# Kernel optimization log

Hardware: AMD Instinct MI355X
Metric: run time of the kernel (lower is better)

Reference implementation:

```python
import jax, jax.numpy as jnp
import numpy as np

G = 8
EPS = 1e-5

def conv3d(x, w, stride=1, padding=0, bias=None):
    out = jax.lax.conv_general_dilated(
        x, w, (stride,) * 3, [(padding, padding)] * 3,
        dimension_numbers=('NCDHW', 'OIDHW', 'NCDHW'))
    if bias is not None:
        out = out + bias.reshape(1, -1, 1, 1, 1)
    return out

def batchnorm(x, g, b):
    mu = x.mean(axis=(0, 2, 3, 4), keepdims=True)
    var = x.var(axis=(0, 2, 3, 4), keepdims=True)
    return (x - mu) * jax.lax.rsqrt(var + EPS) * g.reshape(1, -1, 1, 1, 1) + b.reshape(1, -1, 1, 1, 1)

def up2_trilinear_ac(x):
    # trilinear upsample x2, align_corners=True
    def interp(a, axis):
        n = a.shape[axis]; m = 2 * n
        src = jnp.arange(m, dtype=a.dtype) * ((n - 1) / (m - 1))
        i0 = jnp.floor(src).astype(jnp.int32)
        i1 = jnp.minimum(i0 + 1, n - 1)
        w = src - i0.astype(a.dtype)
        a0 = jnp.take(a, i0, axis=axis)
        a1 = jnp.take(a, i1, axis=axis)
        shp = [1] * a.ndim; shp[axis] = m
        w = w.reshape(shp)
        return a0 * (1 - w) + a1 * w
    for ax in (2, 3, 4):
        x = interp(x, ax)
    return x

def double_conv_up(x, c1, g1, b1, c2, g2, b2):
    x = jax.nn.relu(batchnorm(conv3d(x, c1, padding=1), g1, b1))
    x = up2_trilinear_ac(x)
    x = jax.nn.relu(batchnorm(conv3d(x, c2, padding=1), g2, b2))
    return x

def correlation_3d(prev, nxt):
    # FunctionCorrelation_3D: 3 z-edge-masked copies of prev x 9 (dx,dy) shifts of next
    N, C, X, Y, Z = prev.shape
    zslab = jnp.zeros_like(prev[..., :1])
    pm = [jnp.concatenate([prev[..., :-1], zslab], -1),  # k=-1: last z slice zeroed
          prev,                                          # k=0
          jnp.concatenate([zslab, prev[..., 1:]], -1)]   # k=+1: first z slice zeroed
    npad = jnp.pad(nxt, [(0, 0), (0, 0), (1, 1), (1, 1), (0, 0)])
    ns = [npad[:, :, 1 + di:1 + di + X, 1 + dj:1 + dj + Y, :]
          for di in (-1, 0, 1) for dj in (-1, 0, 1)]
    chans = [(pm[k] * ns[s]).mean(axis=1) for k in range(3) for s in range(9)]
    return jnp.stack(chans, axis=1)  # [N,27,X,Y,Z]

def fwd_diff(a, axis):
    hi = jax.lax.slice_in_dim(a, 1, a.shape[axis], axis=axis)
    zero = jnp.zeros_like(jax.lax.slice_in_dim(a, 0, 1, axis=axis))
    return jnp.concatenate([hi, zero], axis=axis) - a

def cgrid_to_motion(u, v, w, shape):
    mu = 0.5 * (u[:, :, 1:-1, 1:-1, 1:] + u[:, :, 1:-1, 1:-1, :-1])
    mv = 0.5 * (v[:, :, 1:-1, 1:, 1:-1] + v[:, :, 1:-1, :-1, 1:-1])
    mw = 0.5 * (w[:, :, 1:, 1:-1, 1:-1] + w[:, :, :-1, 1:-1, 1:-1])
    m = jnp.concatenate([mu, mv, mw], axis=1)
    H, W, T = shape
    up = (m.shape[2] - H) // 2; left = (m.shape[3] - W) // 2; front = (m.shape[4] - T) // 2
    return m[:, :, up:up + H, left:left + W, front:front + T]

def calc_phi_velocity(phi, shape):
    u = fwd_diff(phi, 4)[:, :, :, :, :-1]
    v = fwd_diff(phi, 3)[:, :, :, :-1, :]
    w = fwd_diff(phi, 2)[:, :, :-1, :, :]
    return cgrid_to_motion(u, v, w, shape)

def calc_stream_velocity(s, shape):
    s0, s1, s2 = s[:, 0:1], s[:, 1:2], s[:, 2:3]
    u = (fwd_diff(s1, 2) - fwd_diff(s0, 3))[:, :, :, :, :-1]
    v = (fwd_diff(s0, 4) - fwd_diff(s2, 2))[:, :, :, :-1, :]
    w = (fwd_diff(s2, 3) - fwd_diff(s1, 4))[:, :, :-1, :, :]
    return cgrid_to_motion(u, v, w, shape)

def trilinear_sample(tex, px, py, pz):
    N, C, X, Y, Z = tex.shape
    px = jnp.clip(px, 0.0, X - 1.0); py = jnp.clip(py, 0.0, Y - 1.0); pz = jnp.clip(pz, 0.0, Z - 1.0)
    x0 = jnp.floor(px).astype(jnp.int32); y0 = jnp.floor(py).astype(jnp.int32); z0 = jnp.floor(pz).astype(jnp.int32)
    x1 = jnp.minimum(x0 + 1, X - 1); y1 = jnp.minimum(y0 + 1, Y - 1); z1 = jnp.minimum(z0 + 1, Z - 1)
    fx = (px - x0.astype(px.dtype))[:, None]
    fy = (py - y0.astype(py.dtype))[:, None]
    fz = (pz - z0.astype(pz.dtype))[:, None]
    tf = tex.reshape(N, C, X * Y * Z)
    def gather(xi, yi, zi):
        idx = ((xi * Y + yi) * Z + zi).reshape(N, 1, -1)
        idx = jnp.broadcast_to(idx, (N, C, X * Y * Z))
        return jnp.take_along_axis(tf, idx, axis=2).reshape(N, C, X, Y, Z)
    c = ((gather(x0, y0, z0) * (1 - fx) + gather(x1, y0, z0) * fx) * (1 - fy)
         + (gather(x0, y1, z0) * (1 - fx) + gather(x1, y1, z0) * fx) * fy) * (1 - fz) \
        + ((gather(x0, y0, z1) * (1 - fx) + gather(x1, y0, z1) * fx) * (1 - fy)
           + (gather(x0, y1, z1) * (1 - fx) + gather(x1, y1, z1) * fx) * fy) * fz
    return c

def bfecc_warp(tex, vel):
    # vel channel 0 -> z (last axis), 1 -> y, 2 -> x displacements
    N, C, X, Y, Z = tex.shape
    gx, gy, gz = jnp.meshgrid(jnp.arange(X, dtype=tex.dtype),
                              jnp.arange(Y, dtype=tex.dtype),
                              jnp.arange(Z, dtype=tex.dtype), indexing='ij')
    def advect(f, v):
        return trilinear_sample(f, gx[None] - v[:, 2], gy[None] - v[:, 1], gz[None] - v[:, 0])
    phi1 = advect(tex, vel)
    phi2 = advect(phi1, -vel)
    return advect(tex + 0.5 * (tex - phi2), vel)

def helm_forward(P):
    prev, nxt, texture = P['prev'], P['next'], P['texture']
    mask, boundary = P['mask'], P['boundary']
    B, C, H, W, T = prev.shape
    shape = texture.shape[-3:]
    pm = (prev * mask).reshape(B * G, C // G, H, W, T)
    pb = (prev * boundary).reshape(B * G, C // G, H, W, T)
    nm = (nxt * mask).reshape(B * G, C // G, H, W, T)
    f_pm = conv3d(pm, P['enc_w'], stride=2, bias=P['enc_b'])
    f_pb = conv3d(pb, P['enc_w'], stride=2, bias=P['enc_b'])
    f_nm = conv3d(nm, P['enc_w'], stride=2, bias=P['enc_b'])
    corr = jnp.concatenate([correlation_3d(f_pm, f_nm), correlation_3d(f_pb, f_nm)], axis=1)
    phi = double_conv_up(corr, P['phi_c1_w'], P['phi_bn1_g'], P['phi_bn1_b'],
                         P['phi_c2_w'], P['phi_bn2_g'], P['phi_bn2_b'])
    phi = conv3d(phi, P['phi_out_w'], bias=P['phi_out_b']) * P['phi_weight']
    vort = double_conv_up(corr, P['vort_c1_w'], P['vort_bn1_g'], P['vort_bn1_b'],
                          P['vort_c2_w'], P['vort_bn2_g'], P['vort_bn2_b'])
    vort = conv3d(vort, P['vort_out_w'], bias=P['vort_out_b']) * P['vort_weight'] * nxt.shape[-2]
    helmholtz = jnp.concatenate([phi, vort], axis=1)  # [B*G,4,H,W,T]
    vel_phi = calc_phi_velocity(helmholtz[:, 0:1], shape)
    vel_vort = calc_stream_velocity(helmholtz[:, 1:4], shape)
    vel = vel_phi + vel_vort
    Bt, Ct, Ht, Wt, Tt = texture.shape
    tex_g = texture.reshape(Bt * G, Ct // G, Ht, Wt, Tt)
    pred = bfecc_warp(tex_g, vel).reshape(Bt, Ct, Ht, Wt, Tt)
    h = jnp.moveaxis(pred, 1, -1)
    mu = h.mean(-1, keepdims=True); var = h.var(-1, keepdims=True)
    h = (h - mu) * jax.lax.rsqrt(var + EPS) * P['ln_g'] + P['ln_b']
    h = jax.nn.gelu(h @ P['ff_w1'] + P['ff_b1'], approximate=False) @ P['ff_w2'] + P['ff_b2']
    x = pred + jnp.moveaxis(h, -1, 1)
    return x, helmholtz, vel, vel_phi, vel_vort

def setup_inputs() -> dict:
    key = jax.random.key(0)
    ks = jax.random.split(key, 16)
    D = 64
    inp = {
        'prev': jax.random.normal(ks[0], (1, D, 66, 66, 66), jnp.float32),
        'next': jax.random.normal(ks[1], (1, D, 66, 66, 66), jnp.float32),
        'texture': jax.random.normal(ks[2], (1, D, 64, 64, 64), jnp.float32),
        'mask': jax.random.uniform(ks[3], (1, 1, 66, 66, 66), jnp.float32),
        'boundary': jax.random.uniform(ks[4], (1, 1, 66, 66, 66), jnp.float32),
        'enc_w': 0.02 * jax.random.normal(ks[5], (D, D // G, 2, 2, 2), jnp.float32),
        'enc_b': jnp.zeros((D,), jnp.float32),
        'phi_c1_w': 0.02 * jax.random.normal(ks[6], (8, 54, 3, 3, 3), jnp.float32),
        'phi_bn1_g': jnp.ones((8,), jnp.float32), 'phi_bn1_b': jnp.zeros((8,), jnp.float32),
        'phi_c2_w': 0.02 * jax.random.normal(ks[7], (8, 8, 3, 3, 3), jnp.float32),
        'phi_bn2_g': jnp.ones((8,), jnp.float32), 'phi_bn2_b': jnp.zeros((8,), jnp.float32),
        'phi_out_w': 0.02 * jax.random.normal(ks[8], (1, 8, 1, 1, 1), jnp.float32),
        'phi_out_b': jnp.zeros((1,), jnp.float32),
        'vort_c1_w': 0.02 * jax.random.normal(ks[9], (8, 54, 3, 3, 3), jnp.float32),
        'vort_bn1_g': jnp.ones((8,), jnp.float32), 'vort_bn1_b': jnp.zeros((8,), jnp.float32),
        'vort_c2_w': 0.02 * jax.random.normal(ks[10], (8, 8, 3, 3, 3), jnp.float32),
        'vort_bn2_g': jnp.ones((8,), jnp.float32), 'vort_bn2_b': jnp.zeros((8,), jnp.float32),
        'vort_out_w': 0.02 * jax.random.normal(ks[11], (3, 8, 1, 1, 1), jnp.float32),
        'vort_out_b': jnp.zeros((3,), jnp.float32),
        'phi_weight': jnp.array([0.5], jnp.float32),
        'vort_weight': jnp.array([0.1], jnp.float32),
        'ln_g': jnp.ones((D,), jnp.float32), 'ln_b': jnp.zeros((D,), jnp.float32),
        'ff_w1': 0.02 * jax.random.normal(ks[12], (D, D), jnp.float32),
        'ff_b1': jnp.zeros((D,), jnp.float32),
        'ff_w2': 0.02 * jax.random.normal(ks[13], (D, D), jnp.float32),
        'ff_b2': jnp.zeros((D,), jnp.float32),
    }
    return inp

def reference(prev, next, texture, mask, boundary, enc_w, enc_b,
              phi_c1_w, phi_bn1_g, phi_bn1_b, phi_c2_w, phi_bn2_g, phi_bn2_b, phi_out_w, phi_out_b,
              vort_c1_w, vort_bn1_g, vort_bn1_b, vort_c2_w, vort_bn2_g, vort_bn2_b, vort_out_w, vort_out_b,
              phi_weight, vort_weight, ln_g, ln_b, ff_w1, ff_b1, ff_w2, ff_b2):
    P = dict(prev=prev, next=next, texture=texture, mask=mask, boundary=boundary,
             enc_w=enc_w, enc_b=enc_b,
             phi_c1_w=phi_c1_w, phi_bn1_g=phi_bn1_g, phi_bn1_b=phi_bn1_b,
             phi_c2_w=phi_c2_w, phi_bn2_g=phi_bn2_g, phi_bn2_b=phi_bn2_b,
             phi_out_w=phi_out_w, phi_out_b=phi_out_b,
             vort_c1_w=vort_c1_w, vort_bn1_g=vort_bn1_g, vort_bn1_b=vort_bn1_b,
             vort_c2_w=vort_c2_w, vort_bn2_g=vort_bn2_g, vort_bn2_b=vort_bn2_b,
             vort_out_w=vort_out_w, vort_out_b=vort_out_b,
             phi_weight=phi_weight, vort_weight=vort_weight,
             ln_g=ln_g, ln_b=ln_b, ff_w1=ff_w1, ff_b1=ff_b1, ff_w2=ff_w2, ff_b2=ff_b2)
    return helm_forward(P)
```

## Files before the change

kernel.cpp:

```cpp
#include <hip/hip_runtime.h>
#include <math.h>

constexpr int S1 = 66, S1_2 = S1*S1, S1_3 = S1*S1*S1;
constexpr int S2 = 33, S2_2 = S2*S2, S2_3 = S2*S2*S2;
constexpr int S3 = 64, S3_2 = S3*S3, S3_3 = S3*S3*S3;
constexpr int NG = 8;
constexpr int CG = 8;
constexpr int D  = 64;

constexpr size_t X_OFF     = 0;
constexpr size_t HELM_OFF  = (size_t)D*S3_3;
constexpr size_t VEL_OFF   = HELM_OFF + (size_t)NG*4*S1_3;
constexpr size_t VPHI_OFF  = VEL_OFF  + (size_t)NG*3*S3_3;
constexpr size_t VVORT_OFF = VPHI_OFF + (size_t)NG*3*S3_3;

constexpr size_t CORR_OFF  = 0;
constexpr size_t C1P_OFF   = CORR_OFF + (size_t)NG*54*S2_3;
constexpr size_t C1V_OFF   = C1P_OFF  + (size_t)NG*8*S2_3;
constexpr size_t STATS_OFF = C1V_OFF  + (size_t)NG*8*S2_3;

constexpr int NBLK_STAT = 256;

__global__ void __launch_bounds__(256)
enc_kernel(const float* __restrict__ in, const float* __restrict__ msk,
           const float* __restrict__ w,  const float* __restrict__ b,
           float* __restrict__ out) {
    int pos = blockIdx.x*256 + threadIdx.x;
    int g = blockIdx.y;
    if (pos >= S2_3) return;
    int x = pos / S2_2, rem = pos % S2_2, y = rem / S2, z = rem % S2;
    int ib = 2*x*S1_2 + 2*y*S1 + 2*z;
    float mv[8];
#pragma unroll
    for (int c = 0; c < 8; ++c) {
        int dx = c>>2, dy = (c>>1)&1, dz = c&1;
        mv[c] = msk[ib + dx*S1_2 + dy*S1 + dz];
    }
    float mi[64];
#pragma unroll
    for (int ic = 0; ic < 8; ++ic) {
        const float* inc = in + (size_t)(g*CG + ic)*S1_3 + ib;
#pragma unroll
        for (int c = 0; c < 8; ++c) {
            int dx = c>>2, dy = (c>>1)&1, dz = c&1;
            mi[ic*8 + c] = inc[dx*S1_2 + dy*S1 + dz] * mv[c];
        }
    }
    for (int oc = 0; oc < 64; ++oc) {
        float acc = b[oc];
#pragma unroll
        for (int t = 0; t < 64; ++t) acc = fmaf(mi[t], w[oc*64 + t], acc);
        out[(size_t)(g*64 + oc)*S2_3 + pos] = acc;
    }
}

__global__ void __launch_bounds__(256)
corr_kernel(const float* __restrict__ fpv, const float* __restrict__ fnv,
            float* __restrict__ corr, int base_ch) {
    int pos = blockIdx.x*256 + threadIdx.x;
    int g = blockIdx.y;
    if (pos >= S2_3) return;
    int x = pos / S2_2, rem = pos % S2_2, y = rem / S2, z = rem % S2;
    const float* fp = fpv + (size_t)g*64*S2_3;
    const float* fn = fnv + (size_t)g*64*S2_3;
    int   nidx[9];
    float nmask[9];
#pragma unroll
    for (int di = -1; di <= 1; ++di) {
        int xx = x + di; int xc = min(max(xx,0),S2-1); bool okx = (unsigned)xx < (unsigned)S2;
#pragma unroll
        for (int dj = -1; dj <= 1; ++dj) {
            int yy = y + dj; int yc = min(max(yy,0),S2-1);
            bool ok = okx && ((unsigned)yy < (unsigned)S2);
            nidx [(di+1)*3 + dj+1] = xc*S2_2 + yc*S2 + z;
            nmask[(di+1)*3 + dj+1] = ok ? 1.f : 0.f;
        }
    }
    float acc[9] = {0,0,0,0,0,0,0,0,0};
    for (int c = 0; c < 64; ++c) {
        float pc = fp[(size_t)c*S2_3 + pos];
        const float* fnc = fn + (size_t)c*S2_3;
#pragma unroll
        for (int s = 0; s < 9; ++s) acc[s] = fmaf(pc, fnc[nidx[s]]*nmask[s], acc[s]);
    }
    const float inv64 = 1.f/64.f;
#pragma unroll
    for (int k = 0; k < 3; ++k) {
        float zf = ((k==0 && z==S2-1) || (k==2 && z==0)) ? 0.f : inv64;
#pragma unroll
        for (int s = 0; s < 9; ++s)
            corr[(size_t)(g*54 + base_ch + k*9 + s)*S2_3 + pos] = acc[s]*zf;
    }
}

template<int NIC, int S_>
__global__ void __launch_bounds__(256)
conv3_kernel(const float* __restrict__ in, const float* __restrict__ w,
             float* __restrict__ out) {
    constexpr int SS = S_*S_, SSS = S_*S_*S_;
    int pos = blockIdx.x*256 + threadIdx.x;
    int g = blockIdx.y;
    if (pos >= SSS) return;
    int x = pos / SS, rem = pos % SS, y = rem / S_, z = rem % S_;
    float acc[8] = {0,0,0,0,0,0,0,0};
    for (int ic = 0; ic < NIC; ++ic) {
        const float* inc = in + (size_t)(g*NIC + ic)*SSS;
        float v[27];
#pragma unroll
        for (int dx = -1; dx <= 1; ++dx) {
            int xx = x + dx; int xc = min(max(xx,0),S_-1); bool okx = (unsigned)xx < (unsigned)S_;
#pragma unroll
            for (int dy = -1; dy <= 1; ++dy) {
                int yy = y + dy; int yc = min(max(yy,0),S_-1);
                bool oky = okx && ((unsigned)yy < (unsigned)S_);
#pragma unroll
                for (int dz = -1; dz <= 1; ++dz) {
                    int zz = z + dz; int zc = min(max(zz,0),S_-1);
                    bool ok = oky && ((unsigned)zz < (unsigned)S_);
                    float t = inc[xc*SS + yc*S_ + zc];
                    v[(dx+1)*9 + (dy+1)*3 + (dz+1)] = ok ? t : 0.f;
                }
            }
        }
#pragma unroll
        for (int oc = 0; oc < 8; ++oc) {
            const float* wr = w + (size_t)(oc*NIC + ic)*27;
#pragma unroll
            for (int t = 0; t < 27; ++t) acc[oc] = fmaf(v[t], wr[t], acc[oc]);
        }
    }
#pragma unroll
    for (int oc = 0; oc < 8; ++oc)
        out[(size_t)(g*8 + oc)*SSS + pos] = acc[oc];
}

__global__ void __launch_bounds__(256)
bn_part_kernel(const float* __restrict__ in, int npos, double* __restrict__ part) {
    int ch = blockIdx.y;
    int blk = blockIdx.x;
    int tid = threadIdx.x;
    double s = 0.0, ss = 0.0;
    for (int g = 0; g < NG; ++g) {
        const float* p = in + (size_t)(g*8 + ch)*npos;
        for (int i = blk*256 + tid; i < npos; i += NBLK_STAT*256) {
            double v = p[i]; s += v; ss += v*v;
        }
    }
    __shared__ double sd[256], sd2[256];
    sd[tid] = s; sd2[tid] = ss; __syncthreads();
    for (int o = 128; o > 0; o >>= 1) {
        if (tid < o) { sd[tid] += sd[tid+o]; sd2[tid] += sd2[tid+o]; }
        __syncthreads();
    }
    if (tid == 0) {
        part[((size_t)ch*NBLK_STAT + blk)*2    ] = sd[0];
        part[((size_t)ch*NBLK_STAT + blk)*2 + 1] = sd2[0];
    }
}

__global__ void __launch_bounds__(256)
bn_finish_kernel(const double* __restrict__ part, int npos, float* __restrict__ stats) {
    int ch = blockIdx.x;
    int tid = threadIdx.x;
    __shared__ double sd[256], sd2[256];
    sd[tid]  = part[((size_t)ch*NBLK_STAT + tid)*2];
    sd2[tid] = part[((size_t)ch*NBLK_STAT + tid)*2 + 1];
    __syncthreads();
    for (int o = 128; o > 0; o >>= 1) {
        if (tid < o) { sd[tid] += sd[tid+o]; sd2[tid] += sd2[tid+o]; }
        __syncthreads();
    }
    if (tid == 0) {
        double n = (double)npos * NG;
        double mean = sd[0]/n;
        double var  = sd2[0]/n - mean*mean;
        stats[ch*2]   = (float)mean;
        stats[ch*2+1] = (float)(1.0/sqrt(var + 1e-5));
    }
}

__global__ void __launch_bounds__(256)
bn_relu_up_kernel(const float* __restrict__ in, const float* __restrict__ stats,
                  const float* __restrict__ gamma, const float* __restrict__ beta,
                  float* __restrict__ out) {
    int pos = blockIdx.x*256 + threadIdx.x;
    if (pos >= S1_3) return;
    int gc = blockIdx.y;
    int ch = gc & 7;
    int X = pos / S1_2, rem = pos % S1_2, Y = rem / S1, Z = rem % S1;
    const float scale = (float)(32.0/65.0);
    float sx = (float)X*scale, sy = (float)Y*scale, sz = (float)Z*scale;
    int x0 = (int)floorf(sx), y0 = (int)floorf(sy), z0 = (int)floorf(sz);
    float wx = sx - (float)x0, wy = sy - (float)y0, wz = sz - (float)z0;
    int x1 = min(x0+1, S2-1), y1 = min(y0+1, S2-1), z1 = min(z0+1, S2-1);
    float a = stats[ch*2+1]*gamma[ch];
    float c = beta[ch] - stats[ch*2]*a;
    const float* p = in + (size_t)gc*S2_3;
    auto val = [&](int xi, int yi, int zi) {
        float t = fmaf(p[xi*S2_2 + yi*S2 + zi], a, c);
        return t > 0.f ? t : 0.f;
    };
    float t00 = val(x0,y0,z0)*(1.f-wx) + val(x1,y0,z0)*wx;
    float t10 = val(x0,y1,z0)*(1.f-wx) + val(x1,y1,z0)*wx;
    float t01 = val(x0,y0,z1)*(1.f-wx) + val(x1,y0,z1)*wx;
    float t11 = val(x0,y1,z1)*(1.f-wx) + val(x1,y1,z1)*wx;
    float u0 = t00*(1.f-wy) + t10*wy;
    float u1 = t01*(1.f-wy) + t11*wy;
    out[(size_t)gc*S1_3 + pos] = u0*(1.f-wz) + u1*wz;
}

template<int NOC>
__global__ void __launch_bounds__(256)
outconv_kernel(const float* __restrict__ in, const float* __restrict__ stats,
               const float* __restrict__ gamma, const float* __restrict__ beta,
               const float* __restrict__ ow, const float* __restrict__ ob,
               const float* __restrict__ wscale, float extra,
               float* __restrict__ helm, int oc_off) {
    int pos = blockIdx.x*256 + threadIdx.x;
    int g = blockIdx.y;
    if (pos >= S1_3) return;
    float r[8];
#pragma unroll
    for (int ic = 0; ic < 8; ++ic) {
        float a = stats[ic*2+1]*gamma[ic];
        float c = beta[ic] - stats[ic*2]*a;
        float t = fmaf(in[(size_t)(g*8 + ic)*S1_3 + pos], a, c);
        r[ic] = t > 0.f ? t : 0.f;
    }
    float sc = wscale[0]*extra;
#pragma unroll
    for (int oc = 0; oc < NOC; ++oc) {
        float acc = ob[oc];
#pragma unroll
        for (int ic = 0; ic < 8; ++ic) acc = fmaf(r[ic], ow[oc*8 + ic], acc);
        helm[(size_t)(g*4 + oc_off + oc)*S1_3 + pos] = acc*sc;
    }
}

__global__ void __launch_bounds__(256)
velocity_kernel(const float* __restrict__ helm, float* __restrict__ vel,
                float* __restrict__ vphi, float* __restrict__ vvort) {
    int pos = blockIdx.x*256 + threadIdx.x;
    int g = blockIdx.y;
    if (pos >= S3_3) return;
    int x = pos / S3_2, rem = pos % S3_2, y = rem / S3, z = rem % S3;
    const float* H = helm + (size_t)g*4*S1_3;
    auto idx = [&](int c, int i, int j, int k) { return (size_t)c*S1_3 + i*S1_2 + j*S1 + k; };
    float pu = 0.5f*(H[idx(0,x+1,y+1,z+2)] - H[idx(0,x+1,y+1,z  )]);
    float pv = 0.5f*(H[idx(0,x+1,y+2,z+1)] - H[idx(0,x+1,y  ,z+1)]);
    float pw = 0.5f*(H[idx(0,x+2,y+1,z+1)] - H[idx(0,x  ,y+1,z+1)]);
    float vu = 0.5f*( (H[idx(2,x+2,y+1,z+1)]-H[idx(2,x+1,y+1,z+1)]) - (H[idx(1,x+1,y+2,z+1)]-H[idx(1,x+1,y+1,z+1)])
                    + (H[idx(2,x+2,y+1,z  )]-H[idx(2,x+1,y+1,z  )]) - (H[idx(1,x+1,y+2,z  )]-H[idx(1,x+1,y+1,z  )]) );
    float vv = 0.5f*( (H[idx(1,x+1,y+1,z+2)]-H[idx(1,x+1,y+1,z+1)]) - (H[idx(3,x+2,y+1,z+1)]-H[idx(3,x+1,y+1,z+1)])
                    + (H[idx(1,x+1,y  ,z+2)]-H[idx(1,x+1,y  ,z+1)]) - (H[idx(3,x+2,y  ,z+1)]-H[idx(3,x+1,y  ,z+1)]) );
    float vw = 0.5f*( (H[idx(3,x+1,y+2,z+1)]-H[idx(3,x+1,y+1,z+1)]) - (H[idx(2,x+1,y+1,z+2)]-H[idx(2,x+1,y+1,z+1)])
                    + (H[idx(3,x  ,y+2,z+1)]-H[idx(3,x  ,y+1,z+1)]) - (H[idx(2,x  ,y+1,z+2)]-H[idx(2,x  ,y+1,z+1)]) );
    size_t o0 = (size_t)(g*3+0)*S3_3 + pos;
    size_t o1 = (size_t)(g*3+1)*S3_3 + pos;
    size_t o2 = (size_t)(g*3+2)*S3_3 + pos;
    vphi[o0] = pu;      vphi[o1] = pv;      vphi[o2] = pw;
    vvort[o0] = vu;     vvort[o1] = vv;     vvort[o2] = vw;
    vel[o0] = pu + vu;  vel[o1] = pv + vv;  vel[o2] = pw + vw;
}

template<bool BFECC>
__global__ void __launch_bounds__(256)
advect_kernel(const float* __restrict__ f, const float* __restrict__ f2,
              const float* __restrict__ vel, float vsign,
              float* __restrict__ out) {
    int pos = blockIdx.x*256 + threadIdx.x;
    int g = blockIdx.y;
    if (pos >= S3_3) return;
    int x = pos / S3_2, rem = pos % S3_2, y = rem / S3, z = rem % S3;
    float px = (float)x - vsign*vel[(size_t)(g*3+2)*S3_3 + pos];
    float py = (float)y - vsign*vel[(size_t)(g*3+1)*S3_3 + pos];
    float pz = (float)z - vsign*vel[(size_t)(g*3+0)*S3_3 + pos];
    px = fminf(fmaxf(px, 0.f), 63.f);
    py = fminf(fmaxf(py, 0.f), 63.f);
    pz = fminf(fmaxf(pz, 0.f), 63.f);
    int x0 = (int)floorf(px), y0 = (int)floorf(py), z0 = (int)floorf(pz);
    int x1 = min(x0+1, S3-1), y1 = min(y0+1, S3-1), z1 = min(z0+1, S3-1);
    float fx = px - (float)x0, fy = py - (float)y0, fz = pz - (float)z0;
    int xo0 = x0*S3_2, xo1 = x1*S3_2, yo0 = y0*S3, yo1 = y1*S3;
    int i000 = xo0+yo0+z0, i100 = xo1+yo0+z0, i010 = xo0+yo1+z0, i110 = xo1+yo1+z0;
    int i001 = xo0+yo0+z1, i101 = xo1+yo0+z1, i011 = xo0+yo1+z1, i111 = xo1+yo1+z1;
    for (int c = 0; c < 8; ++c) {
        const float* fc  = f  + (size_t)(g*8 + c)*S3_3;
        const float* f2c = BFECC ? (f2 + (size_t)(g*8 + c)*S3_3) : nullptr;
        auto corner = [&](int i) {
            float t = fc[i];
            if (BFECC) { float p = f2c[i]; t = t + 0.5f*(t - p); }
            return t;
        };
        float g000 = corner(i000), g100 = corner(i100), g010 = corner(i010), g110 = corner(i110);
        float g001 = corner(i001), g101 = corner(i101), g011 = corner(i011), g111 = corner(i111);
        float r = ((g000*(1.f-fx) + g100*fx)*(1.f-fy) + (g010*(1.f-fx) + g110*fx)*fy)*(1.f-fz)
                + ((g001*(1.f-fx) + g101*fx)*(1.f-fy) + (g011*(1.f-fx) + g111*fx)*fy)*fz;
        out[(size_t)(g*8 + c)*S3_3 + pos] = r;
    }
}

__global__ void __launch_bounds__(256)
ln_mlp_kernel(const float* __restrict__ pred,
              const float* __restrict__ lng, const float* __restrict__ lnb,
              const float* __restrict__ w1, const float* __restrict__ b1,
              const float* __restrict__ w2, const float* __restrict__ b2,
              float* __restrict__ xout) {
    int pos = blockIdx.x*256 + threadIdx.x;
    if (pos >= S3_3) return;
    float s = 0.f, ss = 0.f;
    for (int i = 0; i < 64; ++i) {
        float v = pred[(size_t)i*S3_3 + pos];
        s += v; ss += v*v;
    }
    float mu = s*(1.f/64.f);
    float var = ss*(1.f/64.f) - mu*mu;
    float rs = rsqrtf(var + 1e-5f);
    float y1[64];
#pragma unroll
    for (int j = 0; j < 64; ++j) y1[j] = b1[j];
    for (int i = 0; i < 64; ++i) {
        float v = pred[(size_t)i*S3_3 + pos];
        float hn = (v - mu)*rs*lng[i] + lnb[i];
        const float* wr = w1 + i*64;
#pragma unroll
        for (int j = 0; j < 64; ++j) y1[j] = fmaf(hn, wr[j], y1[j]);
    }
#pragma unroll
    for (int j = 0; j < 64; ++j) {
        float t = y1[j];
        y1[j] = 0.5f*t*(1.f + erff(t*0.70710678118654752f));
    }
    for (int c = 0; c < 64; ++c) {
        float acc = b2[c];
#pragma unroll
        for (int j = 0; j < 64; ++j) acc = fmaf(y1[j], w2[j*64 + c], acc);
        xout[(size_t)c*S3_3 + pos] = pred[(size_t)c*S3_3 + pos] + acc;
    }
}

extern "C" void kernel_launch(void* const* d_in, const int* in_sizes, int n_in,
                              void* d_out, int out_size, void* d_ws, size_t ws_size,
                              hipStream_t stream) {
    const float* prev       = (const float*)d_in[0];
    const float* nxt        = (const float*)d_in[1];
    const float* tex        = (const float*)d_in[2];
    const float* mask       = (const float*)d_in[3];
    const float* boundary   = (const float*)d_in[4];
    const float* enc_w      = (const float*)d_in[5];
    const float* enc_b      = (const float*)d_in[6];
    const float* phi_c1_w   = (const float*)d_in[7];
    const float* phi_bn1_g  = (const float*)d_in[8];
    const float* phi_bn1_b  = (const float*)d_in[9];
    const float* phi_c2_w   = (const float*)d_in[10];
    const float* phi_bn2_g  = (const float*)d_in[11];
    const float* phi_bn2_b  = (const float*)d_in[12];
    const float* phi_out_w  = (const float*)d_in[13];
    const float* phi_out_b  = (const float*)d_in[14];
    const float* vort_c1_w  = (const float*)d_in[15];
    const float* vort_bn1_g = (const float*)d_in[16];
    const float* vort_bn1_b = (const float*)d_in[17];
    const float* vort_c2_w  = (const float*)d_in[18];
    const float* vort_bn2_g = (const float*)d_in[19];
    const float* vort_bn2_b = (const float*)d_in[20];
    const float* vort_out_w = (const float*)d_in[21];
    const float* vort_out_b = (const float*)d_in[22];
    const float* phi_weight = (const float*)d_in[23];
    const float* vort_weight= (const float*)d_in[24];
    const float* ln_g       = (const float*)d_in[25];
    const float* ln_b       = (const float*)d_in[26];
    const float* ff_w1      = (const float*)d_in[27];
    const float* ff_b1      = (const float*)d_in[28];
    const float* ff_w2      = (const float*)d_in[29];
    const float* ff_b2      = (const float*)d_in[30];

    float* ws  = (float*)d_ws;
    float* out = (float*)d_out;

    float* w_corr  = ws + CORR_OFF;
    float* w_c1p   = ws + C1P_OFF;
    float* w_c1v   = ws + C1V_OFF;
    float* w_stats = ws + STATS_OFF;
    float* w_big   = ws;

    float* o_x    = out + X_OFF;
    float* o_helm = out + HELM_OFF;
    float* o_vel  = out + VEL_OFF;
    float* o_vphi = out + VPHI_OFF;
    float* o_vvort= out + VVORT_OFF;

    double* d_part = (double*)o_x;

    dim3 b256(256);
    dim3 gs2((S2_3 + 255)/256, NG);
    dim3 gs1((S1_3 + 255)/256, NG);
    dim3 gs1c((S1_3 + 255)/256, NG*CG);
    dim3 gs3((S3_3 + 255)/256, NG);
    dim3 gmlp((S3_3 + 255)/256);
    dim3 gstat(NBLK_STAT, 8);

    enc_kernel<<<gs2, b256, 0, stream>>>(nxt,  mask,     enc_w, enc_b, o_x);
    enc_kernel<<<gs2, b256, 0, stream>>>(prev, mask,     enc_w, enc_b, o_vel);
    corr_kernel<<<gs2, b256, 0, stream>>>(o_vel, o_x, w_corr, 0);
    enc_kernel<<<gs2, b256, 0, stream>>>(prev, boundary, enc_w, enc_b, o_vel);
    corr_kernel<<<gs2, b256, 0, stream>>>(o_vel, o_x, w_corr, 27);

    conv3_kernel<54,33><<<gs2, b256, 0, stream>>>(w_corr, phi_c1_w,  w_c1p);
    conv3_kernel<54,33><<<gs2, b256, 0, stream>>>(w_corr, vort_c1_w, w_c1v);
    bn_part_kernel  <<<gstat, b256, 0, stream>>>(w_c1p, S2_3, d_part);
    bn_finish_kernel<<<8,     b256, 0, stream>>>(d_part, S2_3, w_stats + 0);
    bn_part_kernel  <<<gstat, b256, 0, stream>>>(w_c1v, S2_3, d_part);
    bn_finish_kernel<<<8,     b256, 0, stream>>>(d_part, S2_3, w_stats + 16);

    bn_relu_up_kernel<<<gs1c, b256, 0, stream>>>(w_c1p, w_stats + 0,  phi_bn1_g,  phi_bn1_b,  o_x);
    bn_relu_up_kernel<<<gs1c, b256, 0, stream>>>(w_c1v, w_stats + 16, vort_bn1_g, vort_bn1_b, o_vel);

    conv3_kernel<8,66><<<gs1, b256, 0, stream>>>(o_x, phi_c2_w, w_big);
    bn_part_kernel  <<<gstat, b256, 0, stream>>>(w_big, S1_3, d_part);
    bn_finish_kernel<<<8,     b256, 0, stream>>>(d_part, S1_3, w_stats + 32);
    outconv_kernel<1><<<gs1, b256, 0, stream>>>(w_big, w_stats + 32, phi_bn2_g, phi_bn2_b,
                                                phi_out_w, phi_out_b, phi_weight, 1.0f,
                                                o_helm, 0);
    conv3_kernel<8,66><<<gs1, b256, 0, stream>>>(o_vel, vort_c2_w, w_big);
    bn_part_kernel  <<<gstat, b256, 0, stream>>>(w_big, S1_3, d_part);
    bn_finish_kernel<<<8,     b256, 0, stream>>>(d_part, S1_3, w_stats + 48);
    outconv_kernel<3><<<gs1, b256, 0, stream>>>(w_big, w_stats + 48, vort_bn2_g, vort_bn2_b,
                                                vort_out_w, vort_out_b, vort_weight, 66.0f,
                                                o_helm, 1);

    velocity_kernel<<<gs3, b256, 0, stream>>>(o_helm, o_vel, o_vphi, o_vvort);

    advect_kernel<false><<<gs3, b256, 0, stream>>>(tex,   nullptr, o_vel,  1.f, w_big);
    advect_kernel<false><<<gs3, b256, 0, stream>>>(w_big, nullptr, o_vel, -1.f, o_x);
    advect_kernel<true ><<<gs3, b256, 0, stream>>>(tex,   o_x,     o_vel,  1.f, w_big);

    ln_mlp_kernel<<<gmlp, b256, 0, stream>>>(w_big, ln_g, ln_b, ff_w1, ff_b1, ff_w2, ff_b2, o_x);
}
```

Measured before the change: 2.884 ms.

## Fuse phi and vort first convs into one LDS-tiled kernel

Replaces the two separate 54-channel 3x3x3 conv launches on the 33^3 correlation volume with one kernel that computes both the phi and vort outputs. Each block stages a 4x8x8 output tile plus halo into shared memory one channel at a time and prefetches the next channel into registers. The correlation input is then read once instead of twice, and the per-thread 27-point global gathers become LDS reads. The cost is 16 accumulators per thread, two barriers per input channel, and tiles that extend past the 33-wide edges and leave some threads idle.

Result: faster. 2.650 ms (-8.1%).

```diff
diff --git a/kernel.cpp b/kernel.cpp
--- a/kernel.cpp
+++ b/kernel.cpp
@@ -90,6 +90,86 @@
 #pragma unroll
         for (int s = 0; s < 9; ++s)
             corr[(size_t)(g*54 + base_ch + k*9 + s)*S2_3 + pos] = acc[s]*zf;
+    }
+}
+
+constexpr int TLX = 4, TLY = 8, TLZ = 8;
+constexpr int NTX = 9, NTY = 5, NTZ = 5;
+constexpr int HLX = TLX+2, HLY = TLY+2, HLZ = TLZ+2;
+constexpr int LZP = 12;
+constexpr int TILE_N = HLX*HLY*LZP;
+
+__global__ void __launch_bounds__(256)
+conv1_fused_kernel(const float* __restrict__ in,
+                   const float* __restrict__ wp,
+                   const float* __restrict__ wv,
+                   float* __restrict__ outp, float* __restrict__ outv) {
+    __shared__ float tile[TILE_N];
+    int tid = threadIdx.x;
+    int g = blockIdx.y;
+    int b = blockIdx.x;
+    int bx = b / (NTY*NTZ), brem = b % (NTY*NTZ), by = brem / NTZ, bz = brem % NTZ;
+    int X0 = bx*TLX, Y0 = by*TLY, Z0 = bz*TLZ;
+    int tx = tid >> 6, ty = (tid >> 3) & 7, tz = tid & 7;
+    int gx = X0 + tx, gy = Y0 + ty, gz = Z0 + tz;
+    bool valid = (gx < S2) && (gy < S2) && (gz < S2);
+    const float* gbase = in + (size_t)g*54*S2_3;
+
+    auto load_ch = [&](int ic, float r[3]) {
+        const float* base = gbase + (size_t)ic*S2_3;
+        int k = 0;
+        for (int i = tid; i < TILE_N; i += 256, ++k) {
+            int lx = i / (HLY*LZP), lr = i % (HLY*LZP), ly = lr / LZP, lz = lr % LZP;
+            int ax = X0-1+lx, ay = Y0-1+ly, az = Z0-1+lz;
+            bool ok = (unsigned)ax < (unsigned)S2 && (unsigned)ay < (unsigned)S2
+                   && (unsigned)az < (unsigned)S2;
+            r[k] = ok ? base[ax*S2_2 + ay*S2 + az] : 0.f;
+        }
+    };
+
+    float accP[8] = {0,0,0,0,0,0,0,0};
+    float accV[8] = {0,0,0,0,0,0,0,0};
+    float r[3];
+    load_ch(0, r);
+
+    for (int ic = 0; ic < 54; ++ic) {
+        __syncthreads();
+        {   int k = 0;
+            for (int i = tid; i < TILE_N; i += 256, ++k) tile[i] = r[k];
+        }
+        float rn[3] = {0.f, 0.f, 0.f};
+        if (ic + 1 < 54) load_ch(ic + 1, rn);
+        __syncthreads();
+
+        float v[27];
+#pragma unroll
+        for (int dx = 0; dx < 3; ++dx)
+#pragma unroll
+            for (int dy = 0; dy < 3; ++dy)
+#pragma unroll
+                for (int dz = 0; dz < 3; ++dz)
+                    v[dx*9 + dy*3 + dz] =
+                        tile[(tx+dx)*(HLY*LZP) + (ty+dy)*LZP + (tz+dz)];
+#pragma unroll
+        for (int oc = 0; oc < 8; ++oc) {
+            const float* wpr = wp + (size_t)(oc*54 + ic)*27;
+            const float* wvr = wv + (size_t)(oc*54 + ic)*27;
+#pragma unroll
+            for (int t = 0; t < 27; ++t) {
+                accP[oc] = fmaf(v[t], wpr[t], accP[oc]);
+                accV[oc] = fmaf(v[t], wvr[t], accV[oc]);
+            }
+        }
+        r[0] = rn[0]; r[1] = rn[1]; r[2] = rn[2];
+    }
+
+    if (valid) {
+        int pos = gx*S2_2 + gy*S2 + gz;
+#pragma unroll
+        for (int oc = 0; oc < 8; ++oc) {
+            outp[(size_t)(g*8 + oc)*S2_3 + pos] = accP[oc];
+            outv[(size_t)(g*8 + oc)*S2_3 + pos] = accV[oc];
+        }
     }
 }
 
@@ -398,6 +478,7 @@
     dim3 gs3((S3_3 + 255)/256, NG);
     dim3 gmlp((S3_3 + 255)/256);
     dim3 gstat(NBLK_STAT, 8);
+    dim3 gc1(NTX*NTY*NTZ, NG);
 
     enc_kernel<<<gs2, b256, 0, stream>>>(nxt,  mask,     enc_w, enc_b, o_x);
     enc_kernel<<<gs2, b256, 0, stream>>>(prev, mask,     enc_w, enc_b, o_vel);
@@ -405,8 +486,8 @@
     enc_kernel<<<gs2, b256, 0, stream>>>(prev, boundary, enc_w, enc_b, o_vel);
     corr_kernel<<<gs2, b256, 0, stream>>>(o_vel, o_x, w_corr, 27);
 
-    conv3_kernel<54,33><<<gs2, b256, 0, stream>>>(w_corr, phi_c1_w,  w_c1p);
-    conv3_kernel<54,33><<<gs2, b256, 0, stream>>>(w_corr, vort_c1_w, w_c1v);
+    conv1_fused_kernel<<<gc1, b256, 0, stream>>>(w_corr, phi_c1_w, vort_c1_w,
+                                                 w_c1p, w_c1v);
     bn_part_kernel  <<<gstat, b256, 0, stream>>>(w_c1p, S2_3, d_part);
     bn_finish_kernel<<<8,     b256, 0, stream>>>(d_part, S2_3, w_stats + 0);
     bn_part_kernel  <<<gstat, b256, 0, stream>>>(w_c1v, S2_3, d_part);
```
